# Performance work log

Measured on AMD Instinct MI355X. Metric: run time of the kernel, lower is better.

Reference implementation:

```python
import jax, jax.numpy as jnp
import numpy as np

N_NODES = 100000
N_EDGES = 20000
NNZ = 1000000
IN_CH = 128
OUT_DIM = 64  # heads(8) * out_channels(8)


def setup_inputs() -> dict:
    key = jax.random.key(0)
    k1, k2, k3, k4, k5, k6 = jax.random.split(key, 6)
    X = jax.random.normal(k1, (N_NODES, IN_CH), dtype=jnp.float32)
    vertex = jax.random.randint(k2, (NNZ,), 0, N_NODES, dtype=jnp.int64)
    edges = jax.random.randint(k3, (NNZ,), 0, N_EDGES, dtype=jnp.int64)
    W_lin = jax.random.normal(k4, (IN_CH, OUT_DIM), dtype=jnp.float32) * (1.0 / np.sqrt(IN_CH))
    degE = jax.random.uniform(k5, (N_EDGES, 1), dtype=jnp.float32)
    degV = jax.random.uniform(k6, (N_NODES, 1), dtype=jnp.float32)
    W_edge = jnp.ones((N_EDGES, 1), dtype=jnp.float32)
    return {"X": X, "vertex": vertex, "edges": edges, "W_lin": W_lin,
            "degE": degE, "degV": degV, "W_edge": W_edge}


def reference(X, vertex, edges, W_lin, degE, degV, W_edge):
    # linear projection (no bias): [N, in] @ [in, heads*out] -> [N, D]
    Xl = X @ W_lin
    # gather node features per incidence, scatter-sum into hyperedges
    Xve = Xl[vertex]                                             # [nnz, D]
    Xe = jax.ops.segment_sum(Xve, edges, num_segments=N_EDGES)   # [E, D]
    Xe = Xe * degE * W_edge                                      # edge degree + weight scaling
    # gather hyperedge features per incidence, scatter-sum back to nodes
    Xev = Xe[edges]                                              # [nnz, D]
    Xv = jax.ops.segment_sum(Xev, vertex, num_segments=N_NODES)  # [N, D]
    return Xv * degV
```

## Files before the change

kernel.cpp:

```cpp
#include <hip/hip_runtime.h>
#include <hip/hip_bf16.h>

typedef __hip_bfloat16 bf16;
__device__ __forceinline__ float bf2f(bf16 v) { return __bfloat162float(v); }

typedef __attribute__((ext_vector_type(8))) short short8;
typedef __attribute__((ext_vector_type(4))) float floatx4;
typedef __attribute__((ext_vector_type(4))) int intx4;

#define EB_BITS 8
#define VB_BITS 10
#define MAXBK   256
#define F1_ITEMS 2048
#define XS_STRIDE 136
#define SMEM_INTS 5892
#define HF_MAXIT 20

__device__ __forceinline__ int rbase(int b, int nEB, int capE, int capV) {
  return (b < nEB) ? b * capE : nEB * capE + (b - nEB) * capV;
}

__device__ void bucketize_body(int* smem4,
    const int* __restrict__ vertex, const int* __restrict__ edges,
    int* __restrict__ gcursor, int* __restrict__ records,
    int nnz, int KB, int nEB, int capE, int capV, int bb) {
  int* cnt    = smem4;
  int* scanEx = smem4 + 256;
  int* bases  = smem4 + 512;
  int* wsum4  = smem4 + 768;
  int* staged = smem4 + 772;
  unsigned char* sbkt = (unsigned char*)(smem4 + 772 + 4096);

  const int tid  = threadIdx.x;
  const int lane = tid & 63;
  const int wid  = tid >> 6;
  const int base = bb * F1_ITEMS;
  const int iEnd = min(nnz, base + F1_ITEMS);

  cnt[tid] = 0;
  __syncthreads();

  int recs[16], bks[16], ps[16];
  const int i0 = base + tid * 8;
  if (i0 + 7 < iEnd) {
    const intx4 ea = __builtin_nontemporal_load((const intx4*)&edges[i0]);
    const intx4 eb = __builtin_nontemporal_load((const intx4*)&edges[i0 + 4]);
    const intx4 va = __builtin_nontemporal_load((const intx4*)&vertex[i0]);
    const intx4 vb = __builtin_nontemporal_load((const intx4*)&vertex[i0 + 4]);
    const int ee[8] = {ea.x, ea.y, ea.z, ea.w, eb.x, eb.y, eb.z, eb.w};
    const int vv[8] = {va.x, va.y, va.z, va.w, vb.x, vb.y, vb.z, vb.w};
#pragma unroll
    for (int j = 0; j < 8; ++j) {
      const int e = ee[j], v = vv[j];
      const int bkE = e >> EB_BITS;
      const int bkV = nEB + (v >> VB_BITS);
      recs[2*j]   = ((e & ((1 << EB_BITS) - 1)) << 17) | v;
      bks[2*j]    = bkE;
      ps[2*j]     = atomicAdd(&cnt[bkE], 1);
      recs[2*j+1] = ((v & ((1 << VB_BITS) - 1)) << 17) | e;
      bks[2*j+1]  = bkV;
      ps[2*j+1]   = atomicAdd(&cnt[bkV], 1);
    }
  } else {
#pragma unroll
    for (int j = 0; j < 8; ++j) {
      const int i = i0 + j;
      if (i < iEnd) {
        const int e = edges[i];
        const int v = vertex[i];
        const int bkE = e >> EB_BITS;
        const int bkV = nEB + (v >> VB_BITS);
        recs[2*j]   = ((e & ((1 << EB_BITS) - 1)) << 17) | v;
        bks[2*j]    = bkE;
        ps[2*j]     = atomicAdd(&cnt[bkE], 1);
        recs[2*j+1] = ((v & ((1 << VB_BITS) - 1)) << 17) | e;
        bks[2*j+1]  = bkV;
        ps[2*j+1]   = atomicAdd(&cnt[bkV], 1);
      } else {
        bks[2*j] = -1;  bks[2*j+1] = -1;
      }
    }
  }
  __syncthreads();

  const int c = cnt[tid];
  int inc = c;
#pragma unroll
  for (int d = 1; d < 64; d <<= 1) {
    int t = __shfl_up(inc, d, 64);
    if (lane >= d) inc += t;
  }
  if (lane == 63) wsum4[wid] = inc;
  __syncthreads();
  if (tid < 4) {
    int wv = wsum4[tid];
#pragma unroll
    for (int d = 1; d < 4; d <<= 1) {
      int t = __shfl_up(wv, d, 64);
      if (tid >= d) wv += t;
    }
    wsum4[tid] = wv;
  }
  __syncthreads();
  const int excl = inc - c + (wid > 0 ? wsum4[wid - 1] : 0);

  if (tid < KB && c > 0)
    bases[tid] = rbase(tid, nEB, capE, capV) + atomicAdd(&gcursor[tid], c);
  scanEx[tid] = excl;
  __syncthreads();

#pragma unroll
  for (int j = 0; j < 16; ++j) {
    if (bks[j] >= 0) {
      const int s = scanEx[bks[j]] + ps[j];
      staged[s] = recs[j];
      sbkt[s] = (unsigned char)bks[j];
    }
  }
  __syncthreads();

  const int nrec = 2 * (iEnd - base);
  for (int s = tid; s < nrec; s += 256) {
    const int b = sbkt[s];
    records[bases[b] + (s - scanEx[b])] = staged[s];
  }
}

__device__ __forceinline__ unsigned int pack_bf16x2(float lo, float hi) {
  bf16 a = __float2bfloat16(lo);
  bf16 b = __float2bfloat16(hi);
  unsigned short ua = *(unsigned short*)&a;
  unsigned short ub = *(unsigned short*)&b;
  return (unsigned int)ua | ((unsigned int)ub << 16);
}

__device__ void gemm_body(int* smem4,
    const float* __restrict__ X, const float* __restrict__ W,
    bf16* __restrict__ Xl, int Nrows, int ntiles, int gb, int GB) {
  unsigned short* S = (unsigned short*)smem4;

  const int tid  = threadIdx.x;
  const int wave = tid >> 6;
  const int lane = tid & 63;
  const int quad = lane >> 4;
  const int l15  = lane & 15;

  for (int i = tid; i < 8192; i += 256) {
    const int k = i >> 6, n = i & 63;
    bf16 h = __float2bfloat16(W[i]);
    S[n * XS_STRIDE + k] = *(unsigned short*)&h;
  }
  __syncthreads();

  short8 bfrag[4][4];
#pragma unroll
  for (int ct = 0; ct < 4; ++ct)
#pragma unroll
    for (int kt = 0; kt < 4; ++kt)
      bfrag[ct][kt] = *(const short8*)&S[(ct * 16 + l15) * XS_STRIDE + kt * 32 + quad * 8];
  __syncthreads();

  const int r  = tid >> 2;
  const int c0 = (tid & 3) * 32;

  for (int tile = gb; tile < ntiles; tile += GB) {
    const int row0 = tile * 64;
    {
      int rr = row0 + r;
      if (rr >= Nrows) rr = Nrows - 1;
      const float* src = X + (size_t)rr * 128 + c0;
      unsigned short* dst = &S[r * XS_STRIDE + c0];
#pragma unroll
      for (int q = 0; q < 4; ++q) {
        const float4 f0 = *(const float4*)(src + q * 8);
        const float4 f1 = *(const float4*)(src + q * 8 + 4);
        uint4 o;
        o.x = pack_bf16x2(f0.x, f0.y);
        o.y = pack_bf16x2(f0.z, f0.w);
        o.z = pack_bf16x2(f1.x, f1.y);
        o.w = pack_bf16x2(f1.z, f1.w);
        *(uint4*)(dst + q * 8) = o;
      }
    }
    __syncthreads();

    const int m = wave * 16 + l15;
    short8 afrag[4];
#pragma unroll
    for (int kt = 0; kt < 4; ++kt)
      afrag[kt] = *(const short8*)&S[m * XS_STRIDE + kt * 32 + quad * 8];

    floatx4 acc[4];
#pragma unroll
    for (int ct = 0; ct < 4; ++ct) {
      acc[ct] = (floatx4){0.f, 0.f, 0.f, 0.f};
#pragma unroll
      for (int kt = 0; kt < 4; ++kt)
        acc[ct] = __builtin_amdgcn_mfma_f32_16x16x32_bf16(
            afrag[kt], bfrag[ct][kt], acc[ct], 0, 0, 0);
    }

    const int rbase_ = row0 + wave * 16 + quad * 4;
#pragma unroll
    for (int ct = 0; ct < 4; ++ct) {
      const int col = ct * 16 + l15;
#pragma unroll
      for (int reg = 0; reg < 4; ++reg) {
        const int row = rbase_ + reg;
        if (row < Nrows) Xl[(size_t)row * 64 + col] = __float2bfloat16(acc[ct][reg]);
      }
    }
    __syncthreads();
  }
}

__global__ __launch_bounds__(256) void fused1_kernel(
    const int* __restrict__ vertex, const int* __restrict__ edges,
    int* __restrict__ gcursor, int* __restrict__ records,
    const float* __restrict__ X, const float* __restrict__ W,
    bf16* __restrict__ Xl,
    int nnz, int KB, int nEB, int capE, int capV, int Nrows, int ntiles, int GB) {
  __shared__ int smem4[SMEM_INTS];
  if ((int)blockIdx.x < GB)
    gemm_body(smem4, X, W, Xl, Nrows, ntiles, blockIdx.x, GB);
  else
    bucketize_body(smem4, vertex, edges, gcursor, records, nnz, KB, nEB,
                   capE, capV, blockIdx.x - GB);
}

__global__ __launch_bounds__(1024) void histfill_kernel(
    const int* __restrict__ records, const int* __restrict__ gcursor,
    int* __restrict__ offs, int* __restrict__ perm,
    int nEB, int capE, int capV, int E, int M, int KB, int totrec) {
  __shared__ int cnt[1 << VB_BITS];
  __shared__ int wsum[16];
  const int b    = blockIdx.x;
  const int tid  = threadIdx.x;
  const int lane = tid & 63;
  const int wid  = tid >> 6;

  const int base = rbase(b, nEB, capE, capV);
  const int end  = base + gcursor[b];

  int bb = 0;
  {
    const int tot = (tid < KB) ? gcursor[tid] : 0;
    int inc = tot;
    if (tid < 256) {
#pragma unroll
      for (int d = 1; d < 64; d <<= 1) {
        const int t = __shfl_up(inc, d, 64);
        if (lane >= d) inc += t;
      }
      if (lane == 63) wsum[wid] = inc;
    }
    __syncthreads();
    if (tid < 256) {
      int wbase = 0;
      for (int w = 0; w < wid; ++w) wbase += wsum[w];
      cnt[tid] = wbase + inc - tot;
    }
    __syncthreads();
    bb = cnt[b];
    __syncthreads();
  }
  if (b == 0 && tid == 0) offs[M] = totrec;

  cnt[tid] = 0;
  __syncthreads();

  int myrec[HF_MAXIT], myp[HF_MAXIT];
#pragma unroll
  for (int it = 0; it < HF_MAXIT / 4; ++it) {
    const int r = base + (tid + it * 1024) * 4;
    if (r + 3 < end) {
      const intx4 rv = __builtin_nontemporal_load((const intx4*)&records[r]);
      myrec[4*it+0] = rv.x;  myp[4*it+0] = atomicAdd(&cnt[rv.x >> 17], 1);
      myrec[4*it+1] = rv.y;  myp[4*it+1] = atomicAdd(&cnt[rv.y >> 17], 1);
      myrec[4*it+2] = rv.z;  myp[4*it+2] = atomicAdd(&cnt[rv.z >> 17], 1);
      myrec[4*it+3] = rv.w;  myp[4*it+3] = atomicAdd(&cnt[rv.w >> 17], 1);
    } else {
#pragma unroll
      for (int k = 0; k < 4; ++k) {
        const int rr = r + k;
        if (rr < end) {
          const int rec = records[rr];
          myrec[4*it+k] = rec;
          myp[4*it+k] = atomicAdd(&cnt[rec >> 17], 1);
        } else {
          myrec[4*it+k] = -1;
        }
      }
    }
  }
  __syncthreads();

  const int c = cnt[tid];
  int inc = c;
#pragma unroll
  for (int d = 1; d < 64; d <<= 1) {
    const int t = __shfl_up(inc, d, 64);
    if (lane >= d) inc += t;
  }
  if (lane == 63) wsum[wid] = inc;
  __syncthreads();
  if (tid < 16) {
    int wv = wsum[tid];
#pragma unroll
    for (int d = 1; d < 16; d <<= 1) {
      const int t = __shfl_up(wv, d, 64);
      if (tid >= d) wv += t;
    }
    wsum[tid] = wv;
  }
  __syncthreads();
  const int goff = bb + inc - c + (wid > 0 ? wsum[wid - 1] : 0);

  int seg_lo, segN;
  if (b < nEB) { seg_lo = b << EB_BITS;               segN = min(E - seg_lo, 1 << EB_BITS); }
  else         { seg_lo = E + ((b - nEB) << VB_BITS); segN = min(M - seg_lo, 1 << VB_BITS); }
  if (tid < segN) offs[seg_lo + tid] = goff;
  cnt[tid] = goff;
  __syncthreads();

#pragma unroll
  for (int it = 0; it < HF_MAXIT; ++it) {
    if (myrec[it] >= 0)
      perm[cnt[myrec[it] >> 17] + myp[it]] = myrec[it] & 0x1FFFF;
  }
}

__global__ __launch_bounds__(256) void gather_e_kernel(
    const bf16* __restrict__ Xl, const int* __restrict__ perm,
    const int* __restrict__ offs, const float* __restrict__ degE,
    const float* __restrict__ W_edge, bf16* __restrict__ Xe, int E) {
  const int gtid = blockIdx.x * 256 + threadIdx.x;
  const int e    = gtid >> 6;
  const int lane = gtid & 63;
  if (e >= E) return;

  const int beg = offs[e];
  const int end = offs[e + 1];
  float acc = 0.f;

  for (int base = beg; base < end; base += 64) {
    const int n = min(64, end - base);
    const int idx = (lane < n) ? perm[base + lane] : 0;
    int jj = 0;
    for (; jj + 4 <= n; jj += 4) {
      const int v0 = __shfl(idx, jj + 0, 64);
      const int v1 = __shfl(idx, jj + 1, 64);
      const int v2 = __shfl(idx, jj + 2, 64);
      const int v3 = __shfl(idx, jj + 3, 64);
      const float f0 = bf2f(Xl[(size_t)v0 * 64 + lane]);
      const float f1 = bf2f(Xl[(size_t)v1 * 64 + lane]);
      const float f2 = bf2f(Xl[(size_t)v2 * 64 + lane]);
      const float f3 = bf2f(Xl[(size_t)v3 * 64 + lane]);
      acc += (f0 + f1) + (f2 + f3);
    }
    for (; jj < n; ++jj) {
      const int v = __shfl(idx, jj, 64);
      acc += bf2f(Xl[(size_t)v * 64 + lane]);
    }
  }
  const float s = degE[e] * W_edge[e];
  Xe[(size_t)e * 64 + lane] = __float2bfloat16(acc * s);
}

__global__ __launch_bounds__(256) void gather_v_kernel(
    const bf16* __restrict__ Xe, const int* __restrict__ perm,
    const int* __restrict__ offs, const float* __restrict__ degV,
    float* __restrict__ out, int N, int E) {
  const int gtid = blockIdx.x * 256 + threadIdx.x;
  const int v    = gtid >> 6;
  const int lane = gtid & 63;
  if (v >= N) return;

  const int beg = offs[E + v];
  const int end = offs[E + v + 1];
  float acc = 0.f;

  for (int base = beg; base < end; base += 64) {
    const int n = min(64, end - base);
    const int idx = (lane < n) ? perm[base + lane] : 0;
    int jj = 0;
    for (; jj + 4 <= n; jj += 4) {
      const int e0 = __shfl(idx, jj + 0, 64);
      const int e1 = __shfl(idx, jj + 1, 64);
      const int e2 = __shfl(idx, jj + 2, 64);
      const int e3 = __shfl(idx, jj + 3, 64);
      const float f0 = bf2f(Xe[(size_t)e0 * 64 + lane]);
      const float f1 = bf2f(Xe[(size_t)e1 * 64 + lane]);
      const float f2 = bf2f(Xe[(size_t)e2 * 64 + lane]);
      const float f3 = bf2f(Xe[(size_t)e3 * 64 + lane]);
      acc += (f0 + f1) + (f2 + f3);
    }
    for (; jj < n; ++jj) {
      const int e = __shfl(idx, jj, 64);
      acc += bf2f(Xe[(size_t)e * 64 + lane]);
    }
  }
  __builtin_nontemporal_store(acc * degV[v], &out[(size_t)v * 64 + lane]);
}

extern "C" void kernel_launch(void* const* d_in, const int* in_sizes, int n_in,
                              void* d_out, int out_size, void* d_ws, size_t ws_size,
                              hipStream_t stream) {
  const float* X      = (const float*)d_in[0];
  const int*   vertex = (const int*)d_in[1];
  const int*   edges  = (const int*)d_in[2];
  const float* W      = (const float*)d_in[3];
  const float* degE   = (const float*)d_in[4];
  const float* degV   = (const float*)d_in[5];
  const float* W_edge = (const float*)d_in[6];
  float* out = (float*)d_out;

  const int nnz = in_sizes[1];
  const int E   = in_sizes[4];
  const int N   = in_sizes[5];
  const int M   = E + N;

  const int nEB = (E + (1 << EB_BITS) - 1) >> EB_BITS;
  const int nVB = (N + (1 << VB_BITS) - 1) >> VB_BITS;
  const int KB  = nEB + nVB;

  int capE = (nnz / nEB) * 3 / 2 + 256;
  int capV = (nnz / nVB) * 3 / 2 + 256;
  if (capE > HF_MAXIT * 1024) capE = HF_MAXIT * 1024;
  if (capV > HF_MAXIT * 1024) capV = HF_MAXIT * 1024;
  capE = (capE + 3) & ~3;
  capV = (capV + 3) & ~3;
  const size_t rec_total = (size_t)nEB * capE + (size_t)nVB * capV;

  char* p = (char*)d_ws;
  auto alloc = [&](size_t bytes) -> void* {
    void* r = (void*)p;
    p += (bytes + 255) & ~(size_t)255;
    return r;
  };
  int*  offs    = (int*)alloc((size_t)(M + 1) * 4);
  int*  gcursor = (int*)alloc(MAXBK * 4);
  int*  perm    = (int*)alloc((size_t)2 * nnz * 4);
  int*  records = (int*)alloc(rec_total * 4);
  bf16* Xl      = (bf16*)alloc((size_t)N * 64 * 2);
  bf16* Xe      = (bf16*)alloc((size_t)E * 64 * 2);

  const int f1blocks = (nnz + F1_ITEMS - 1) / F1_ITEMS;
  const int ntiles   = (N + 63) / 64;
  const int GB       = ntiles < 512 ? ntiles : 512;

  hipMemsetAsync(gcursor, 0, MAXBK * 4, stream);
  fused1_kernel<<<GB + f1blocks, 256, 0, stream>>>(
      vertex, edges, gcursor, records, X, W, Xl,
      nnz, KB, nEB, capE, capV, N, ntiles, GB);
  histfill_kernel<<<KB, 1024, 0, stream>>>(records, gcursor, offs, perm,
                                           nEB, capE, capV, E, M, KB, 2 * nnz);
  gather_e_kernel<<<(E + 3) / 4, 256, 0, stream>>>(Xl, perm, offs, degE, W_edge, Xe, E);
  gather_v_kernel<<<(N + 3) / 4, 256, 0, stream>>>(Xe, perm, offs, degV, out, N, E);
}
```

Measured before the change: 108.9 us.

## Split fused GEMM/bucketize kernel into separate launches and halve bucketize chunk

Splits the fused kernel, whose blocks did either the GEMM or the bucketize work, into separate bucketize and GEMM kernels. The GEMM now runs after histfill instead of alongside bucketize. Each bucketize block now handles 1024 items instead of 2048, which gives more blocks with less shared memory each, and the memset is replaced by a tiny zeroing kernel. This removes the shared-memory sizing coupling between the two workloads and may raise bucketize occupancy. In exchange it adds launches and gives up the overlap of GEMM with bucketize, and smaller chunks mean more global atomics on the cursors.

```diff
diff --git a/kernel.cpp b/kernel.cpp
--- a/kernel.cpp
+++ b/kernel.cpp
@@ -11,47 +11,48 @@
 #define EB_BITS 8
 #define VB_BITS 10
 #define MAXBK   256
-#define F1_ITEMS 2048
+#define F1_ITEMS 1024
 #define XS_STRIDE 136
-#define SMEM_INTS 5892
 #define HF_MAXIT 20
 
 __device__ __forceinline__ int rbase(int b, int nEB, int capE, int capV) {
   return (b < nEB) ? b * capE : nEB * capE + (b - nEB) * capV;
 }
 
-__device__ void bucketize_body(int* smem4,
+__global__ void zero_gc_kernel(int* __restrict__ gcursor) {
+  gcursor[threadIdx.x] = 0;
+}
+
+__global__ __launch_bounds__(256) void bucketize_kernel(
     const int* __restrict__ vertex, const int* __restrict__ edges,
     int* __restrict__ gcursor, int* __restrict__ records,
-    int nnz, int KB, int nEB, int capE, int capV, int bb) {
-  int* cnt    = smem4;
-  int* scanEx = smem4 + 256;
-  int* bases  = smem4 + 512;
-  int* wsum4  = smem4 + 768;
-  int* staged = smem4 + 772;
-  unsigned char* sbkt = (unsigned char*)(smem4 + 772 + 4096);
+    int nnz, int KB, int nEB, int capE, int capV) {
+  __shared__ int cnt[256];
+  __shared__ int scanEx[256];
+  __shared__ int bases[256];
+  __shared__ int wsum4[4];
+  __shared__ int staged[2 * F1_ITEMS];
+  __shared__ unsigned char sbkt[2 * F1_ITEMS];
 
   const int tid  = threadIdx.x;
   const int lane = tid & 63;
   const int wid  = tid >> 6;
-  const int base = bb * F1_ITEMS;
+  const int base = blockIdx.x * F1_ITEMS;
   const int iEnd = min(nnz, base + F1_ITEMS);
 
   cnt[tid] = 0;
   __syncthreads();
 
-  int recs[16], bks[16], ps[16];
-  const int i0 = base + tid * 8;
-  if (i0 + 7 < iEnd) {
-    const intx4 ea = __builtin_nontemporal_load((const intx4*)&edges[i0]);
-    const intx4 eb = __builtin_nontemporal_load((const intx4*)&edges[i0 + 4]);
-    const intx4 va = __builtin_nontemporal_load((const intx4*)&vertex[i0]);
-    const intx4 vb = __builtin_nontemporal_load((const intx4*)&vertex[i0 + 4]);
-    const int ee[8] = {ea.x, ea.y, ea.z, ea.w, eb.x, eb.y, eb.z, eb.w};
-    const int vv[8] = {va.x, va.y, va.z, va.w, vb.x, vb.y, vb.z, vb.w};
-#pragma unroll
-    for (int j = 0; j < 8; ++j) {
-      const int e = ee[j], v = vv[j];
+  int recs[8], bks[8], ps[8];
+  const int i0 = base + tid * 4;
+  if (i0 + 3 < iEnd) {
+    const intx4 ev = __builtin_nontemporal_load((const intx4*)&edges[i0]);
+    const intx4 vv = __builtin_nontemporal_load((const intx4*)&vertex[i0]);
+    const int ee[4] = {ev.x, ev.y, ev.z, ev.w};
+    const int vx[4] = {vv.x, vv.y, vv.z, vv.w};
+#pragma unroll
+    for (int j = 0; j < 4; ++j) {
+      const int e = ee[j], v = vx[j];
       const int bkE = e >> EB_BITS;
       const int bkV = nEB + (v >> VB_BITS);
       recs[2*j]   = ((e & ((1 << EB_BITS) - 1)) << 17) | v;
@@ -63,7 +64,7 @@
     }
   } else {
 #pragma unroll
-    for (int j = 0; j < 8; ++j) {
+    for (int j = 0; j < 4; ++j) {
       const int i = i0 + j;
       if (i < iEnd) {
         const int e = edges[i];
@@ -110,7 +111,7 @@
   __syncthreads();
 
 #pragma unroll
-  for (int j = 0; j < 16; ++j) {
+  for (int j = 0; j < 8; ++j) {
     if (bks[j] >= 0) {
       const int s = scanEx[bks[j]] + ps[j];
       staged[s] = recs[j];
@@ -134,10 +135,10 @@
   return (unsigned int)ua | ((unsigned int)ub << 16);
 }
 
-__device__ void gemm_body(int* smem4,
+__global__ __launch_bounds__(256) void gemm_kernel(
     const float* __restrict__ X, const float* __restrict__ W,
-    bf16* __restrict__ Xl, int Nrows, int ntiles, int gb, int GB) {
-  unsigned short* S = (unsigned short*)smem4;
+    bf16* __restrict__ Xl, int Nrows, int ntiles) {
+  __shared__ unsigned short S[64 * XS_STRIDE];
 
   const int tid  = threadIdx.x;
   const int wave = tid >> 6;
@@ -163,7 +164,7 @@
   const int r  = tid >> 2;
   const int c0 = (tid & 3) * 32;
 
-  for (int tile = gb; tile < ntiles; tile += GB) {
+  for (int tile = blockIdx.x; tile < ntiles; tile += gridDim.x) {
     const int row0 = tile * 64;
     {
       int rr = row0 + r;
@@ -212,20 +213,6 @@
     }
     __syncthreads();
   }
-}
-
-__global__ __launch_bounds__(256) void fused1_kernel(
-    const int* __restrict__ vertex, const int* __restrict__ edges,
-    int* __restrict__ gcursor, int* __restrict__ records,
-    const float* __restrict__ X, const float* __restrict__ W,
-    bf16* __restrict__ Xl,
-    int nnz, int KB, int nEB, int capE, int capV, int Nrows, int ntiles, int GB) {
-  __shared__ int smem4[SMEM_INTS];
-  if ((int)blockIdx.x < GB)
-    gemm_body(smem4, X, W, Xl, Nrows, ntiles, blockIdx.x, GB);
-  else
-    bucketize_body(smem4, vertex, edges, gcursor, records, nnz, KB, nEB,
-                   capE, capV, blockIdx.x - GB);
 }
 
 __global__ __launch_bounds__(1024) void histfill_kernel(
@@ -449,12 +436,12 @@
   const int ntiles   = (N + 63) / 64;
   const int GB       = ntiles < 512 ? ntiles : 512;
 
-  hipMemsetAsync(gcursor, 0, MAXBK * 4, stream);
-  fused1_kernel<<<GB + f1blocks, 256, 0, stream>>>(
-      vertex, edges, gcursor, records, X, W, Xl,
-      nnz, KB, nEB, capE, capV, N, ntiles, GB);
+  zero_gc_kernel<<<1, MAXBK, 0, stream>>>(gcursor);
+  bucketize_kernel<<<f1blocks, 256, 0, stream>>>(vertex, edges, gcursor, records,
+                                                 nnz, KB, nEB, capE, capV);
   histfill_kernel<<<KB, 1024, 0, stream>>>(records, gcursor, offs, perm,
                                            nEB, capE, capV, E, M, KB, 2 * nnz);
+  gemm_kernel<<<GB, 256, 0, stream>>>(X, W, Xl, N, ntiles);
   gather_e_kernel<<<(E + 3) / 4, 256, 0, stream>>>(Xl, perm, offs, degE, W_edge, Xe, E);
   gather_v_kernel<<<(N + 3) / 4, 256, 0, stream>>>(Xe, perm, offs, degV, out, N, E);
 }
```

Result: slower. 124.6 us (+14.5%).
